# Kernel tuning notes

Measured on AMD Instinct MI355X. Metric: run time of the kernel, lower is better.

## Reference

```python
import jax, jax.numpy as jnp
import numpy as np

N_X = 32640   # total xlmr subword tokens (64 seqs x 510 tokens)
N_S = 16320   # total stanza word tokens (2 subwords per word)
E = 65280     # dependency edges (bidirectional, avg degree ~4)
D = 768
GCN_DIM = 256
GCN_NUM = 2
POS_DIM = 4
N_UPOS = 17
N_LABEL = 5


def setup_inputs() -> dict:
    key = jax.random.key(0)
    ks = jax.random.split(key, 8)
    x = jax.random.normal(ks[0], (N_X, D), dtype=jnp.float32)
    # mapStanza2Xlmr as segment ids: xlmr token j belongs to stanza word j//2
    seg = jnp.arange(N_X, dtype=jnp.int32) // 2
    edge_index = jax.random.randint(ks[1], (2, E), 0, N_S, dtype=jnp.int32)
    upos_ids = jax.random.randint(ks[2], (N_S,), 0, N_UPOS, dtype=jnp.int32)
    Wc = jax.random.normal(ks[3], (D, GCN_DIM), dtype=jnp.float32) * 0.02
    bc = jnp.zeros((GCN_DIM,), dtype=jnp.float32)
    gcn_W = jax.random.normal(ks[4], (GCN_NUM, GCN_DIM, GCN_DIM), dtype=jnp.float32) * 0.05
    gcn_b = jnp.zeros((GCN_NUM, GCN_DIM), dtype=jnp.float32)
    upos_table = jax.random.normal(ks[5], (N_UPOS, POS_DIM), dtype=jnp.float32)
    Wcls = jax.random.normal(ks[6], (D + GCN_DIM + POS_DIM, N_LABEL), dtype=jnp.float32) * 0.02
    bcls = jnp.zeros((N_LABEL,), dtype=jnp.float32)
    return {"x": x, "seg": seg, "edge_index": edge_index, "upos_ids": upos_ids,
            "Wc": Wc, "bc": bc, "gcn_W": gcn_W, "gcn_b": gcn_b,
            "upos_table": upos_table, "Wcls": Wcls, "bcls": bcls}


def _gcn_conv(h, srcs, dsts, W, b, n):
    # PyG GCNConv: h' = D^-1/2 (A+I) D^-1/2 (h W) + b  (self loops already in srcs/dsts)
    h = h @ W
    deg = jax.ops.segment_sum(jnp.ones_like(dsts, h.dtype), dsts, num_segments=n)
    dinv = jax.lax.rsqrt(deg)  # deg >= 1 because of self loops
    coef = dinv[srcs] * dinv[dsts]
    out = jax.ops.segment_sum(h[srcs] * coef[:, None], dsts, num_segments=n)
    return out + b


def reference(x, seg, edge_index, upos_ids, Wc, bc, gcn_W, gcn_b, upos_table, Wcls, bcls):
    # mapStanza2Xlmr: mean-pool subword embeddings into stanza word embeddings
    cnt = jax.ops.segment_sum(jnp.ones((N_X,), x.dtype), seg, num_segments=N_S)
    stanza = jax.ops.segment_sum(x, seg, num_segments=N_S) / cnt[:, None]  # [N_S, D]
    # GCN over dependency edges (gcn_mode=0: biedges)
    h = stanza @ Wc + bc
    self_idx = jnp.arange(N_S, dtype=edge_index.dtype)
    srcs = jnp.concatenate([edge_index[0], self_idx])
    dsts = jnp.concatenate([edge_index[1], self_idx])
    for i in range(GCN_NUM):
        h = jax.nn.relu(_gcn_conv(h, srcs, dsts, gcn_W[i], gcn_b[i], N_S))
    # POS embedding + concat + relu
    pos = upos_table[upos_ids]                                  # [N_S, POS_DIM]
    info = jax.nn.relu(jnp.concatenate([h, pos], axis=1))       # [N_S, GCN_DIM+POS_DIM]
    # mapXlmr2Stanza: each subword gathers its (single) word's info
    append = info[seg]                                          # [N_X, GCN_DIM+POS_DIM]
    tok = jnp.concatenate([x, append], axis=1)                  # [N_X, 1028]
    logits = jax.nn.relu(tok) @ Wcls + bcls
    return jax.nn.log_softmax(logits, axis=1)
```

## Files before the change

### kernel.cpp

```cpp
#include <hip/hip_runtime.h>

#define NXT 32640
#define NS  16320
#define NE  65280
#define DD  768
#define GD  256
#define NLAB 5
#define CAP 32

typedef __attribute__((ext_vector_type(8))) short bf16x8;
typedef __attribute__((ext_vector_type(8))) unsigned short u16x8;
typedef __attribute__((ext_vector_type(4))) float f32x4;

__device__ inline unsigned short f2b(float f) {
    unsigned int u = __float_as_uint(f);
    unsigned int r = (u + 0x7FFFu + ((u >> 16) & 1u)) >> 16;
    return (unsigned short)r;
}
__device__ inline float b2f(unsigned short h) {
    return __uint_as_float((unsigned int)h << 16);
}

__device__ inline void tile_transpose(const float* __restrict__ src, unsigned short* __restrict__ dst,
                                      int K, int k0, int n0, int tid) {
    __shared__ unsigned short tl[64][65];
#pragma unroll
    for (int i = 0; i < 16; ++i) {
        int idx = tid + i * 256;
        int r = idx >> 6, c = idx & 63;
        tl[r][c] = f2b(src[(size_t)(k0 + r) * GD + n0 + c]);
    }
    __syncthreads();
#pragma unroll
    for (int i = 0; i < 16; ++i) {
        int idx = tid + i * 256;
        int rr = idx >> 6, cc = idx & 63;
        dst[(size_t)(n0 + rr) * K + k0 + cc] = tl[cc][rr];
    }
}

__global__ void k_setup(int* __restrict__ cnt,
                        const float* __restrict__ Wc, unsigned short* __restrict__ WcT,
                        const float* __restrict__ gcn_W, unsigned short* __restrict__ WT,
                        const float* __restrict__ Wcls, unsigned short* __restrict__ WclsF,
                        const float* __restrict__ upos_table, const float* __restrict__ bcls,
                        float* __restrict__ posLogit) {
    int b = blockIdx.x, t = threadIdx.x;
    if (b < 64) {
        int i = b * 256 + t;
        if (i < NS) cnt[i] = 0;
    } else if (b < 112) {
        int tile = b - 64;
        tile_transpose(Wc, WcT, DD, (tile >> 2) * 64, (tile & 3) * 64, t);
    } else if (b < 128) {
        int tile = b - 112;
        tile_transpose(gcn_W, WT, GD, (tile >> 2) * 64, (tile & 3) * 64, t);
    } else if (b < 144) {
        int tile = b - 128;
        tile_transpose(gcn_W + (size_t)GD * GD, WT + (size_t)GD * GD, GD,
                       (tile >> 2) * 64, (tile & 3) * 64, t);
    } else if (b < 192) {
        int idx = (b - 144) * 256 + t;
        int i = idx & 7, l = (idx >> 3) & 63, s = idx >> 9;
        int col = l & 15;
        int k = s * 32 + (l >> 4) * 8 + i;
        WclsF[idx] = (col < NLAB) ? f2b(Wcls[(size_t)k * NLAB + col]) : 0;
    } else {
        if (t < 17 * NLAB) {
            int u = t / NLAB, l = t - u * NLAB;
            float a = bcls[l];
#pragma unroll
            for (int p = 0; p < 4; ++p) {
                float pv = upos_table[u * 4 + p];
                pv = pv > 0.f ? pv : 0.f;
                a += pv * Wcls[(size_t)(DD + GD + p) * NLAB + l];
            }
            posLogit[t] = a;
        }
    }
}

__global__ __launch_bounds__(256) void k_mega0(const float* __restrict__ x,
                                               const unsigned short* __restrict__ WcT,
                                               const unsigned short* __restrict__ WclsF,
                                               const float* __restrict__ bc,
                                               const int* __restrict__ ei,
                                               int* __restrict__ cnt, int* __restrict__ csr_src,
                                               unsigned short* __restrict__ h_bf,
                                               float* __restrict__ partial) {
    __shared__ unsigned short lds[3584 * 8];
    const int tid = threadIdx.x;
    if (blockIdx.x >= 255) {
        int e = (blockIdx.x - 255) * 256 + tid;
        if (e < NE) {
            int dst = ei[NE + e];
            int slot = atomicAdd(&cnt[dst], 1);
            if (slot < CAP) csr_src[(size_t)dst * CAP + slot] = ei[e];
        }
        return;
    }
    const int lane = tid & 63;
    const int wv   = tid >> 6;
    const int wr   = wv >> 1, wc = wv & 1;
    const int bm   = blockIdx.x * 64;

    const int g = tid >> 6, kc = (tid >> 4) & 3, rl = tid & 15;
    const int w_loc = g * 16 + rl;
    const float* xr0 = x + (size_t)(2 * (bm + w_loc)) * DD + kc * 8;
    const float* xr1 = xr0 + DD;
    const int t0 = 2 * w_loc, t1 = t0 + 1;
    const int ap0 = (t0 >> 4) * 64 + kc * 16 + (t0 & 15);
    const int ap1 = (t1 >> 4) * 64 + kc * 16 + (t1 & 15);
    const unsigned short* srcB = WcT + (size_t)(g * 16 + rl) * DD + kc * 8;

    const bf16x8* ldsv = (const bf16x8*)lds;
    f32x4 acc[2][8] = {};
    f32x4 acc_lg[2] = {};

    for (int it = 0; it < 12; ++it) {
        const int k0 = it * 64;
#pragma unroll
        for (int nh = 0; nh < 4; ++nh)
#pragma unroll
            for (int kh = 0; kh < 2; ++kh)
                __builtin_amdgcn_global_load_lds(srcB + (size_t)nh * 64 * DD + k0 + kh * 32,
                                                 lds + (size_t)(1536 + (nh * 2 + kh) * 256 + tid) * 8,
                                                 16, 0, 0);
#pragma unroll
        for (int kh = 0; kh < 2; ++kh) {
            f32x4 v0a = *(const f32x4*)(xr0 + k0 + kh * 32);
            f32x4 v0b = *(const f32x4*)(xr0 + k0 + kh * 32 + 4);
            f32x4 v1a = *(const f32x4*)(xr1 + k0 + kh * 32);
            f32x4 v1b = *(const f32x4*)(xr1 + k0 + kh * 32 + 4);
            u16x8 pool, ra, rb;
#pragma unroll
            for (int i = 0; i < 4; ++i) {
                pool[i]     = f2b((v0a[i] + v1a[i]) * 0.5f);
                pool[4 + i] = f2b((v0b[i] + v1b[i]) * 0.5f);
                ra[i]     = f2b(v0a[i] > 0.f ? v0a[i] : 0.f);
                ra[4 + i] = f2b(v0b[i] > 0.f ? v0b[i] : 0.f);
                rb[i]     = f2b(v1a[i] > 0.f ? v1a[i] : 0.f);
                rb[4 + i] = f2b(v1b[i] > 0.f ? v1b[i] : 0.f);
            }
            *(u16x8*)(lds + (size_t)(kh * 256 + tid) * 8) = pool;
            *(u16x8*)(lds + (size_t)(512 + kh * 512 + ap0) * 8) = ra;
            *(u16x8*)(lds + (size_t)(512 + kh * 512 + ap1) * 8) = rb;
        }
        __syncthreads();
#pragma unroll
        for (int kh = 0; kh < 2; ++kh) {
            bf16x8 a0 = ldsv[kh * 256 + (wr * 2 + 0) * 64 + lane];
            bf16x8 a1 = ldsv[kh * 256 + (wr * 2 + 1) * 64 + lane];
            bf16x8 at0 = ldsv[512 + kh * 512 + (wv * 2 + 0) * 64 + lane];
            bf16x8 at1 = ldsv[512 + kh * 512 + (wv * 2 + 1) * 64 + lane];
            bf16x8 bl = *(const bf16x8*)(WclsF + (size_t)(it * 2 + kh) * 512 + lane * 8);
            acc_lg[0] = __builtin_amdgcn_mfma_f32_16x16x32_bf16(at0, bl, acc_lg[0], 0, 0, 0);
            acc_lg[1] = __builtin_amdgcn_mfma_f32_16x16x32_bf16(at1, bl, acc_lg[1], 0, 0, 0);
#pragma unroll
            for (int n = 0; n < 8; ++n) {
                bf16x8 b = ldsv[1536 + ((wc * 2 + (n >> 2)) * 2 + kh) * 256 + (n & 3) * 64 + lane];
                acc[0][n] = __builtin_amdgcn_mfma_f32_16x16x32_bf16(a0, b, acc[0][n], 0, 0, 0);
                acc[1][n] = __builtin_amdgcn_mfma_f32_16x16x32_bf16(a1, b, acc[1][n], 0, 0, 0);
            }
        }
        __syncthreads();
    }

    const int rl2 = lane & 15, rq = lane >> 4;
#pragma unroll
    for (int m = 0; m < 2; ++m) {
        int row0 = bm + wr * 32 + m * 16 + rq * 4;
#pragma unroll
        for (int n = 0; n < 8; ++n) {
            int col = wc * 128 + n * 16 + rl2;
            float bv = bc[col];
#pragma unroll
            for (int r = 0; r < 4; ++r)
                h_bf[(size_t)(row0 + r) * GD + col] = f2b(acc[m][n][r] + bv);
        }
    }
    if (rl2 < NLAB) {
#pragma unroll
        for (int tf = 0; tf < 2; ++tf) {
            int tok0 = 2 * bm + wv * 32 + tf * 16 + rq * 4;
#pragma unroll
            for (int r = 0; r < 4; ++r)
                partial[(size_t)(tok0 + r) * NLAB + rl2] = acc_lg[tf][r];
        }
    }
}

__global__ __launch_bounds__(256) void k_gemm(const unsigned short* __restrict__ A,
                                              const unsigned short* __restrict__ BT,
                                              const float* __restrict__ bias,
                                              unsigned short* __restrict__ out,
                                              int K, int nbn) {
    __shared__ unsigned short lds[1536 * 8];
    const int tid  = threadIdx.x;
    const int lane = tid & 63;
    const int wv   = tid >> 6;
    const int wr   = wv >> 1, wc = wv & 1;
    const int bm   = (blockIdx.x / nbn) * 64;
    const int bn   = (blockIdx.x % nbn) * 128;

    const int g  = tid >> 6, w_ = tid & 63, kc = w_ >> 4, rl = w_ & 15;
    const unsigned short* srcA  = A  + (size_t)(bm + g * 16 + rl) * K + kc * 8;
    const unsigned short* srcB0 = BT + (size_t)(bn      + g * 16 + rl) * K + kc * 8;
    const unsigned short* srcB1 = BT + (size_t)(bn + 64 + g * 16 + rl) * K + kc * 8;

    unsigned short* dA0 = lds + (size_t)tid * 8;
    unsigned short* dA1 = dA0 + 256 * 8;
    unsigned short* dB  = lds + (size_t)(512 + tid) * 8;

    const bf16x8* fA = (const bf16x8*)lds + (wr * 2) * 64 + lane;
    const bf16x8* fB = (const bf16x8*)lds + 512 + wc * 256 + lane;

    f32x4 acc[2][4] = {};
    for (int k0 = 0; k0 < K; k0 += 64) {
        __builtin_amdgcn_global_load_lds(srcA  + k0,      dA0,            16, 0, 0);
        __builtin_amdgcn_global_load_lds(srcA  + k0 + 32, dA1,            16, 0, 0);
        __builtin_amdgcn_global_load_lds(srcB0 + k0,      dB,             16, 0, 0);
        __builtin_amdgcn_global_load_lds(srcB1 + k0,      dB + 256 * 8,   16, 0, 0);
        __builtin_amdgcn_global_load_lds(srcB0 + k0 + 32, dB + 512 * 8,   16, 0, 0);
        __builtin_amdgcn_global_load_lds(srcB1 + k0 + 32, dB + 768 * 8,   16, 0, 0);
        __syncthreads();
#pragma unroll
        for (int kh = 0; kh < 2; ++kh) {
            bf16x8 a0 = fA[kh * 256], a1 = fA[kh * 256 + 64];
            const bf16x8* fb = fB + kh * 512;
            bf16x8 b0 = fb[0], b1 = fb[64], b2 = fb[128], b3 = fb[192];
            acc[0][0] = __builtin_amdgcn_mfma_f32_16x16x32_bf16(a0, b0, acc[0][0], 0, 0, 0);
            acc[0][1] = __builtin_amdgcn_mfma_f32_16x16x32_bf16(a0, b1, acc[0][1], 0, 0, 0);
            acc[0][2] = __builtin_amdgcn_mfma_f32_16x16x32_bf16(a0, b2, acc[0][2], 0, 0, 0);
            acc[0][3] = __builtin_amdgcn_mfma_f32_16x16x32_bf16(a0, b3, acc[0][3], 0, 0, 0);
            acc[1][0] = __builtin_amdgcn_mfma_f32_16x16x32_bf16(a1, b0, acc[1][0], 0, 0, 0);
            acc[1][1] = __builtin_amdgcn_mfma_f32_16x16x32_bf16(a1, b1, acc[1][1], 0, 0, 0);
            acc[1][2] = __builtin_amdgcn_mfma_f32_16x16x32_bf16(a1, b2, acc[1][2], 0, 0, 0);
            acc[1][3] = __builtin_amdgcn_mfma_f32_16x16x32_bf16(a1, b3, acc[1][3], 0, 0, 0);
        }
        __syncthreads();
    }

    const int rl2 = lane & 15, rq = lane >> 4;
#pragma unroll
    for (int m = 0; m < 2; ++m) {
        int row0 = bm + wr * 32 + m * 16 + rq * 4;
#pragma unroll
        for (int n = 0; n < 4; ++n) {
            int col = bn + wc * 64 + n * 16 + rl2;
            float bv = bias ? bias[col] : 0.f;
#pragma unroll
            for (int r = 0; r < 4; ++r)
                out[(size_t)(row0 + r) * GD + col] = f2b(acc[m][n][r] + bv);
        }
    }
}

__global__ void k_gather(const int* __restrict__ cnt, const int* __restrict__ csr_src,
                         const unsigned short* __restrict__ hW,
                         const float* __restrict__ b, unsigned short* __restrict__ hout) {
    int w    = blockIdx.x * 4 + (threadIdx.x >> 6);
    int lane = threadIdx.x & 63;
    int c = cnt[w];
    float dw = rsqrtf((float)c + 1.0f);
    const int* sl = csr_src + (size_t)w * CAP;
    float ax = 0.f, ay = 0.f, az = 0.f, aw = 0.f;
    for (int j = 0; j < c; ++j) {
        int src = sl[j];
        float cf = rsqrtf((float)cnt[src] + 1.0f) * dw;
        ushort4 v = *(const ushort4*)&hW[(size_t)src * GD + lane * 4];
        ax += cf * b2f(v.x); ay += cf * b2f(v.y); az += cf * b2f(v.z); aw += cf * b2f(v.w);
    }
    ushort4 sv = *(const ushort4*)&hW[(size_t)w * GD + lane * 4];
    f32x4 bv = *(const f32x4*)&b[lane * 4];
    float c2 = dw * dw;
    float rx = ax + b2f(sv.x) * c2 + bv[0];
    float ry = ay + b2f(sv.y) * c2 + bv[1];
    float rz = az + b2f(sv.z) * c2 + bv[2];
    float rw = aw + b2f(sv.w) * c2 + bv[3];
    ushort4 o;
    o.x = f2b(rx > 0.f ? rx : 0.f);
    o.y = f2b(ry > 0.f ? ry : 0.f);
    o.z = f2b(rz > 0.f ? rz : 0.f);
    o.w = f2b(rw > 0.f ? rw : 0.f);
    *(ushort4*)&hout[(size_t)w * GD + lane * 4] = o;
}

__global__ void k_gather_final(const int* __restrict__ cnt, const int* __restrict__ csr_src,
                               const unsigned short* __restrict__ hW,
                               const float* __restrict__ b,
                               const float* __restrict__ partial,
                               const int* __restrict__ upos_ids,
                               const float* __restrict__ posLogit,
                               const float* __restrict__ Wcls,
                               float* __restrict__ out) {
    int w    = blockIdx.x * 4 + (threadIdx.x >> 6);
    int lane = threadIdx.x & 63;
    int c = cnt[w];
    float dw = rsqrtf((float)c + 1.0f);
    const int* sl = csr_src + (size_t)w * CAP;
    float ax = 0.f, ay = 0.f, az = 0.f, aw = 0.f;
    for (int j = 0; j < c; ++j) {
        int src = sl[j];
        float cf = rsqrtf((float)cnt[src] + 1.0f) * dw;
        ushort4 v = *(const ushort4*)&hW[(size_t)src * GD + lane * 4];
        ax += cf * b2f(v.x); ay += cf * b2f(v.y); az += cf * b2f(v.z); aw += cf * b2f(v.w);
    }
    ushort4 sv = *(const ushort4*)&hW[(size_t)w * GD + lane * 4];
    f32x4 bv = *(const f32x4*)&b[lane * 4];
    float c2 = dw * dw;
    float hv[4];
    hv[0] = ax + b2f(sv.x) * c2 + bv[0];
    hv[1] = ay + b2f(sv.y) * c2 + bv[1];
    hv[2] = az + b2f(sv.z) * c2 + bv[2];
    hv[3] = aw + b2f(sv.w) * c2 + bv[3];
    float acc[NLAB] = {};
#pragma unroll
    for (int i = 0; i < 4; ++i) {
        float v = hv[i] > 0.f ? hv[i] : 0.f;
        const float* wr = Wcls + (size_t)(DD + lane * 4 + i) * NLAB;
#pragma unroll
        for (int l = 0; l < NLAB; ++l) acc[l] += v * wr[l];
    }
#pragma unroll
    for (int off = 32; off > 0; off >>= 1)
#pragma unroll
        for (int l = 0; l < NLAB; ++l) acc[l] += __shfl_xor(acc[l], off);
    if (lane == 0) {
        const float* pl = posLogit + (size_t)upos_ids[w] * NLAB;
        const float* pp = partial + (size_t)w * 2 * NLAB;
#pragma unroll
        for (int t = 0; t < 2; ++t) {
            float lg[NLAB];
#pragma unroll
            for (int l = 0; l < NLAB; ++l) lg[l] = acc[l] + pp[t * NLAB + l] + pl[l];
            float m = lg[0];
#pragma unroll
            for (int l = 1; l < NLAB; ++l) m = fmaxf(m, lg[l]);
            float s = 0.f;
#pragma unroll
            for (int l = 0; l < NLAB; ++l) s += __expf(lg[l] - m);
            float lse = __logf(s) + m;
            float* op = out + (size_t)(2 * w + t) * NLAB;
#pragma unroll
            for (int l = 0; l < NLAB; ++l) op[l] = lg[l] - lse;
        }
    }
}

extern "C" void kernel_launch(void* const* d_in, const int* in_sizes, int n_in,
                              void* d_out, int out_size, void* d_ws, size_t ws_size,
                              hipStream_t stream) {
    const float* x          = (const float*)d_in[0];
    const int*   ei         = (const int*)d_in[2];
    const int*   upos_ids   = (const int*)d_in[3];
    const float* Wc         = (const float*)d_in[4];
    const float* bc         = (const float*)d_in[5];
    const float* gcn_W      = (const float*)d_in[6];
    const float* gcn_b      = (const float*)d_in[7];
    const float* upos_table = (const float*)d_in[8];
    const float* Wcls       = (const float*)d_in[9];
    const float* bcls       = (const float*)d_in[10];
    float* out = (float*)d_out;

    char* ws = (char*)d_ws;
    float* partial          = (float*)ws;            ws += (size_t)NXT * NLAB * 4;
    float* posLogit         = (float*)ws;            ws += (size_t)17 * NLAB * 4;
    unsigned short* h_bf    = (unsigned short*)ws;   ws += (size_t)NS * GD * 2;
    unsigned short* hW_bf   = (unsigned short*)ws;   ws += (size_t)NS * GD * 2;
    unsigned short* WcT     = (unsigned short*)ws;   ws += (size_t)DD * GD * 2;
    unsigned short* WT      = (unsigned short*)ws;   ws += (size_t)2 * GD * GD * 2;
    unsigned short* WclsF   = (unsigned short*)ws;   ws += (size_t)24 * 512 * 2;
    int* cnt                = (int*)ws;              ws += (size_t)NS * 4;
    int* csr_src            = (int*)ws;              ws += (size_t)NS * CAP * 4;

    k_setup<<<193, 256, 0, stream>>>(cnt, Wc, WcT, gcn_W, WT, Wcls, WclsF,
                                     upos_table, bcls, posLogit);
    k_mega0<<<510, 256, 0, stream>>>(x, WcT, WclsF, bc, ei, cnt, csr_src, h_bf, partial);
    k_gemm<<<(NS / 64) * 2, 256, 0, stream>>>(h_bf, WT, nullptr, hW_bf, GD, 2);
    k_gather<<<NS / 4, 256, 0, stream>>>(cnt, csr_src, hW_bf, gcn_b, h_bf);
    k_gemm<<<(NS / 64) * 2, 256, 0, stream>>>(h_bf, WT + (size_t)GD * GD, nullptr, hW_bf, GD, 2);
    k_gather_final<<<NS / 4, 256, 0, stream>>>(cnt, csr_src, hW_bf, gcn_b + GD,
                                               partial, upos_ids, posLogit, Wcls, out);
}
```

Baseline: 115.0 us.

## Widen fused pool+projection kernel to 512 threads and compute logit partials in FP32 FMA

The first fused kernel now runs 512-thread blocks with 8 waves, each wave owning a 64-column slice of the Wc projection. Each thread loads 8 contiguous floats per row pair instead of two 4-float halves. The x-part classifier logits are no longer a padded bf16 MFMA over relu(x); they are computed with scalar FP32 FMAs against a transposed FP32 Wcls, then reduced by shuffles and an LDS combine across wave pairs. This drops the relu-tile LDS staging and the 16-wide MFMA padding in exchange for more VALU work and an extra sync, and it shrinks LDS per block.

```diff
diff --git a/kernel.cpp b/kernel.cpp
--- a/kernel.cpp
+++ b/kernel.cpp
@@ -11,6 +11,7 @@
 typedef __attribute__((ext_vector_type(8))) short bf16x8;
 typedef __attribute__((ext_vector_type(8))) unsigned short u16x8;
 typedef __attribute__((ext_vector_type(4))) float f32x4;
+typedef __attribute__((ext_vector_type(8))) float f32x8;
 
 __device__ inline unsigned short f2b(float f) {
     unsigned int u = __float_as_uint(f);
@@ -42,7 +43,7 @@
 __global__ void k_setup(int* __restrict__ cnt,
                         const float* __restrict__ Wc, unsigned short* __restrict__ WcT,
                         const float* __restrict__ gcn_W, unsigned short* __restrict__ WT,
-                        const float* __restrict__ Wcls, unsigned short* __restrict__ WclsF,
+                        const float* __restrict__ Wcls, float* __restrict__ WclsT,
                         const float* __restrict__ upos_table, const float* __restrict__ bcls,
                         float* __restrict__ posLogit) {
     int b = blockIdx.x, t = threadIdx.x;
@@ -59,12 +60,12 @@
         int tile = b - 128;
         tile_transpose(gcn_W + (size_t)GD * GD, WT + (size_t)GD * GD, GD,
                        (tile >> 2) * 64, (tile & 3) * 64, t);
-    } else if (b < 192) {
+    } else if (b < 159) {
         int idx = (b - 144) * 256 + t;
-        int i = idx & 7, l = (idx >> 3) & 63, s = idx >> 9;
-        int col = l & 15;
-        int k = s * 32 + (l >> 4) * 8 + i;
-        WclsF[idx] = (col < NLAB) ? f2b(Wcls[(size_t)k * NLAB + col]) : 0;
+        if (idx < NLAB * DD) {
+            int l = idx / DD, k = idx - l * DD;
+            WclsT[idx] = Wcls[(size_t)k * NLAB + l];
+        }
     } else {
         if (t < 17 * NLAB) {
             int u = t / NLAB, l = t - u * NLAB;
@@ -80,18 +81,18 @@
     }
 }
 
-__global__ __launch_bounds__(256) void k_mega0(const float* __restrict__ x,
-                                               const unsigned short* __restrict__ WcT,
-                                               const unsigned short* __restrict__ WclsF,
-                                               const float* __restrict__ bc,
-                                               const int* __restrict__ ei,
-                                               int* __restrict__ cnt, int* __restrict__ csr_src,
-                                               unsigned short* __restrict__ h_bf,
-                                               float* __restrict__ partial) {
-    __shared__ unsigned short lds[3584 * 8];
+__global__ __launch_bounds__(512, 2) void k_mega0(const float* __restrict__ x,
+                                                  const unsigned short* __restrict__ WcT,
+                                                  const float* __restrict__ WclsT,
+                                                  const float* __restrict__ bc,
+                                                  const int* __restrict__ ei,
+                                                  int* __restrict__ cnt, int* __restrict__ csr_src,
+                                                  unsigned short* __restrict__ h_bf,
+                                                  float* __restrict__ partial) {
+    __shared__ unsigned short lds[2560 * 8];
     const int tid = threadIdx.x;
     if (blockIdx.x >= 255) {
-        int e = (blockIdx.x - 255) * 256 + tid;
+        int e = (blockIdx.x - 255) * 512 + tid;
         if (e < NE) {
             int dst = ei[NE + e];
             int slot = atomicAdd(&cnt[dst], 1);
@@ -101,64 +102,60 @@
     }
     const int lane = tid & 63;
     const int wv   = tid >> 6;
-    const int wr   = wv >> 1, wc = wv & 1;
+    const int wr   = wv >> 2, wc = wv & 3;
     const int bm   = blockIdx.x * 64;
 
-    const int g = tid >> 6, kc = (tid >> 4) & 3, rl = tid & 15;
+    const int g = tid >> 7, kc = (tid >> 4) & 7, rl = tid & 15;
     const int w_loc = g * 16 + rl;
     const float* xr0 = x + (size_t)(2 * (bm + w_loc)) * DD + kc * 8;
     const float* xr1 = xr0 + DD;
-    const int t0 = 2 * w_loc, t1 = t0 + 1;
-    const int ap0 = (t0 >> 4) * 64 + kc * 16 + (t0 & 15);
-    const int ap1 = (t1 >> 4) * 64 + kc * 16 + (t1 & 15);
-    const unsigned short* srcB = WcT + (size_t)(g * 16 + rl) * DD + kc * 8;
+    const int aw_slot = (kc >> 2) * 256 + g * 64 + (kc & 3) * 16 + rl;
+    const float* wcl = WclsT + kc * 8;
+
+    const unsigned short* srcB[4];
+#pragma unroll
+    for (int q = 0; q < 4; ++q) {
+        int slot = q * 512 + tid;
+        int gran = slot >> 8, chunk = slot & 255;
+        int nh = gran >> 1, kh = gran & 1;
+        int rg = chunk >> 6, kc2 = (chunk >> 4) & 3, rl2 = chunk & 15;
+        srcB[q] = WcT + (size_t)(nh * 64 + rg * 16 + rl2) * DD + kh * 32 + kc2 * 8;
+    }
 
     const bf16x8* ldsv = (const bf16x8*)lds;
-    f32x4 acc[2][8] = {};
-    f32x4 acc_lg[2] = {};
+    f32x4 acc[2][4] = {};
+    float lg0[NLAB] = {}, lg1[NLAB] = {};
 
     for (int it = 0; it < 12; ++it) {
         const int k0 = it * 64;
 #pragma unroll
-        for (int nh = 0; nh < 4; ++nh)
-#pragma unroll
-            for (int kh = 0; kh < 2; ++kh)
-                __builtin_amdgcn_global_load_lds(srcB + (size_t)nh * 64 * DD + k0 + kh * 32,
-                                                 lds + (size_t)(1536 + (nh * 2 + kh) * 256 + tid) * 8,
-                                                 16, 0, 0);
-#pragma unroll
-        for (int kh = 0; kh < 2; ++kh) {
-            f32x4 v0a = *(const f32x4*)(xr0 + k0 + kh * 32);
-            f32x4 v0b = *(const f32x4*)(xr0 + k0 + kh * 32 + 4);
-            f32x4 v1a = *(const f32x4*)(xr1 + k0 + kh * 32);
-            f32x4 v1b = *(const f32x4*)(xr1 + k0 + kh * 32 + 4);
-            u16x8 pool, ra, rb;
-#pragma unroll
-            for (int i = 0; i < 4; ++i) {
-                pool[i]     = f2b((v0a[i] + v1a[i]) * 0.5f);
-                pool[4 + i] = f2b((v0b[i] + v1b[i]) * 0.5f);
-                ra[i]     = f2b(v0a[i] > 0.f ? v0a[i] : 0.f);
-                ra[4 + i] = f2b(v0b[i] > 0.f ? v0b[i] : 0.f);
-                rb[i]     = f2b(v1a[i] > 0.f ? v1a[i] : 0.f);
-                rb[4 + i] = f2b(v1b[i] > 0.f ? v1b[i] : 0.f);
+        for (int q = 0; q < 4; ++q)
+            __builtin_amdgcn_global_load_lds(srcB[q] + k0, lds + (size_t)(512 + q * 512 + tid) * 8, 16, 0, 0);
+        f32x8 va = *(const f32x8*)(xr0 + k0);
+        f32x8 vb = *(const f32x8*)(xr1 + k0);
+        u16x8 pool;
+#pragma unroll
+        for (int i = 0; i < 8; ++i) pool[i] = f2b((va[i] + vb[i]) * 0.5f);
+        *(u16x8*)(lds + (size_t)aw_slot * 8) = pool;
+#pragma unroll
+        for (int l = 0; l < NLAB; ++l) {
+            f32x8 wv8 = *(const f32x8*)(wcl + (size_t)l * DD + k0);
+#pragma unroll
+            for (int i = 0; i < 8; ++i) {
+                float ra = va[i] > 0.f ? va[i] : 0.f;
+                float rb = vb[i] > 0.f ? vb[i] : 0.f;
+                lg0[l] += ra * wv8[i];
+                lg1[l] += rb * wv8[i];
             }
-            *(u16x8*)(lds + (size_t)(kh * 256 + tid) * 8) = pool;
-            *(u16x8*)(lds + (size_t)(512 + kh * 512 + ap0) * 8) = ra;
-            *(u16x8*)(lds + (size_t)(512 + kh * 512 + ap1) * 8) = rb;
         }
         __syncthreads();
 #pragma unroll
         for (int kh = 0; kh < 2; ++kh) {
             bf16x8 a0 = ldsv[kh * 256 + (wr * 2 + 0) * 64 + lane];
             bf16x8 a1 = ldsv[kh * 256 + (wr * 2 + 1) * 64 + lane];
-            bf16x8 at0 = ldsv[512 + kh * 512 + (wv * 2 + 0) * 64 + lane];
-            bf16x8 at1 = ldsv[512 + kh * 512 + (wv * 2 + 1) * 64 + lane];
-            bf16x8 bl = *(const bf16x8*)(WclsF + (size_t)(it * 2 + kh) * 512 + lane * 8);
-            acc_lg[0] = __builtin_amdgcn_mfma_f32_16x16x32_bf16(at0, bl, acc_lg[0], 0, 0, 0);
-            acc_lg[1] = __builtin_amdgcn_mfma_f32_16x16x32_bf16(at1, bl, acc_lg[1], 0, 0, 0);
-#pragma unroll
-            for (int n = 0; n < 8; ++n) {
-                bf16x8 b = ldsv[1536 + ((wc * 2 + (n >> 2)) * 2 + kh) * 256 + (n & 3) * 64 + lane];
+#pragma unroll
+            for (int n = 0; n < 4; ++n) {
+                bf16x8 b = ldsv[512 + (wc * 2 + kh) * 256 + n * 64 + lane];
                 acc[0][n] = __builtin_amdgcn_mfma_f32_16x16x32_bf16(a0, b, acc[0][n], 0, 0, 0);
                 acc[1][n] = __builtin_amdgcn_mfma_f32_16x16x32_bf16(a1, b, acc[1][n], 0, 0, 0);
             }
@@ -171,21 +168,35 @@
     for (int m = 0; m < 2; ++m) {
         int row0 = bm + wr * 32 + m * 16 + rq * 4;
 #pragma unroll
-        for (int n = 0; n < 8; ++n) {
-            int col = wc * 128 + n * 16 + rl2;
+        for (int n = 0; n < 4; ++n) {
+            int col = wc * 64 + n * 16 + rl2;
             float bv = bc[col];
 #pragma unroll
             for (int r = 0; r < 4; ++r)
                 h_bf[(size_t)(row0 + r) * GD + col] = f2b(acc[m][n][r] + bv);
         }
     }
-    if (rl2 < NLAB) {
-#pragma unroll
-        for (int tf = 0; tf < 2; ++tf) {
-            int tok0 = 2 * bm + wv * 32 + tf * 16 + rq * 4;
-#pragma unroll
-            for (int r = 0; r < 4; ++r)
-                partial[(size_t)(tok0 + r) * NLAB + rl2] = acc_lg[tf][r];
+
+#pragma unroll
+    for (int l = 0; l < NLAB; ++l) {
+        lg0[l] += __shfl_xor(lg0[l], 16); lg0[l] += __shfl_xor(lg0[l], 32);
+        lg1[l] += __shfl_xor(lg1[l], 16); lg1[l] += __shfl_xor(lg1[l], 32);
+    }
+    float* comb = (float*)lds;
+    if ((wv & 1) == 0 && lane < 16) {
+        float* cp = comb + (size_t)(g * 16 + lane) * 10;
+#pragma unroll
+        for (int l = 0; l < NLAB; ++l) { cp[l] = lg0[l]; cp[NLAB + l] = lg1[l]; }
+    }
+    __syncthreads();
+    if ((wv & 1) == 1 && lane < 16) {
+        int w = bm + g * 16 + lane;
+        const float* cp = comb + (size_t)(g * 16 + lane) * 10;
+        float* pp = partial + (size_t)w * 2 * NLAB;
+#pragma unroll
+        for (int l = 0; l < NLAB; ++l) {
+            pp[l]        = cp[l] + lg0[l];
+            pp[NLAB + l] = cp[NLAB + l] + lg1[l];
         }
     }
 }
@@ -365,18 +376,18 @@
 
     char* ws = (char*)d_ws;
     float* partial          = (float*)ws;            ws += (size_t)NXT * NLAB * 4;
+    float* WclsT            = (float*)ws;            ws += (size_t)NLAB * DD * 4;
     float* posLogit         = (float*)ws;            ws += (size_t)17 * NLAB * 4;
     unsigned short* h_bf    = (unsigned short*)ws;   ws += (size_t)NS * GD * 2;
     unsigned short* hW_bf   = (unsigned short*)ws;   ws += (size_t)NS * GD * 2;
     unsigned short* WcT     = (unsigned short*)ws;   ws += (size_t)DD * GD * 2;
     unsigned short* WT      = (unsigned short*)ws;   ws += (size_t)2 * GD * GD * 2;
-    unsigned short* WclsF   = (unsigned short*)ws;   ws += (size_t)24 * 512 * 2;
     int* cnt                = (int*)ws;              ws += (size_t)NS * 4;
     int* csr_src            = (int*)ws;              ws += (size_t)NS * CAP * 4;
 
-    k_setup<<<193, 256, 0, stream>>>(cnt, Wc, WcT, gcn_W, WT, Wcls, WclsF,
+    k_setup<<<160, 256, 0, stream>>>(cnt, Wc, WcT, gcn_W, WT, Wcls, WclsT,
                                      upos_table, bcls, posLogit);
-    k_mega0<<<510, 256, 0, stream>>>(x, WcT, WclsF, bc, ei, cnt, csr_src, h_bf, partial);
+    k_mega0<<<510, 512, 0, stream>>>(x, WcT, WclsT, bc, ei, cnt, csr_src, h_bf, partial);
     k_gemm<<<(NS / 64) * 2, 256, 0, stream>>>(h_bf, WT, nullptr, hW_bf, GD, 2);
     k_gather<<<NS / 4, 256, 0, stream>>>(cnt, csr_src, hW_bf, gcn_b, h_bf);
     k_gemm<<<(NS / 64) * 2, 256, 0, stream>>>(h_bf, WT + (size_t)GD * GD, nullptr, hW_bf, GD, 2);
```

Measured after the change: 119.2 us. 3.7% more time.
